# Performance work log

Measured on AMD Instinct MI355X. Metric: run time of the kernel, lower is better.

The kernel has to match this reference:

```python
import jax, jax.numpy as jnp
import numpy as np

EPS = 1e-5


def setup_inputs() -> dict:
    key = jax.random.key(0)
    k1, k2, k3 = jax.random.split(key, 3)
    B, n_per, C_in, C_out = 8, 131072, 32, 64
    N = B * n_per
    coord = jax.random.uniform(k1, (N, 3), dtype=jnp.float32)          # points in unit cube
    feat = jax.random.normal(k2, (N, C_in), dtype=jnp.float32)
    offset = (jnp.arange(1, B + 1, dtype=jnp.int32) * n_per)           # cumulative counts
    W = jax.random.normal(k3, (C_in, C_out), dtype=jnp.float32) * 0.05  # fc weight (no bias)
    gamma = jnp.ones((C_out,), dtype=jnp.float32)
    beta = jnp.zeros((C_out,), dtype=jnp.float32)
    return {"coord": coord, "feat": feat, "offset": offset, "W": W,
            "gamma": gamma, "beta": beta, "grid_size": 0.05}


def reference(coord, feat, offset, W, gamma, beta, grid_size):
    N = coord.shape[0]
    B = offset.shape[0]
    # offset2batch: point i belongs to batch = first b with i < offset[b]
    batch = jnp.searchsorted(offset, jnp.arange(N, dtype=offset.dtype), side="right").astype(jnp.int32)

    # fc -> BatchNorm (training-mode batch stats, biased var) -> ReLU
    h = feat @ W                                                        # [N, C_out]
    mean = h.mean(axis=0)
    var = jnp.mean((h - mean) ** 2, axis=0)
    h = jax.nn.relu((h - mean) * jax.lax.rsqrt(var + EPS) * gamma + beta)

    # start = per-batch min coord (segment_csr 'min' over batch pointer)
    start = jax.ops.segment_min(coord, batch, num_segments=B)           # [B, 3]

    # voxel_grid: integer voxel coords per point, combined with batch into a unique key
    v = jnp.floor((coord - start[batch]) / grid_size).astype(jnp.int32)  # [N, 3] >= 0
    D = v.max(axis=0) + 1                                               # grid extents
    vkey = ((batch * D[0] + v[:, 0]) * D[1] + v[:, 1]) * D[2] + v[:, 2]

    # unique(sorted) + inverse + counts; then segment mean/max by cluster
    uniq, inverse, counts = jnp.unique(vkey, return_inverse=True, return_counts=True)
    inverse = inverse.reshape(-1).astype(jnp.int32)
    M = uniq.shape[0]
    coord_out = jax.ops.segment_sum(coord, inverse, num_segments=M) / counts[:, None].astype(coord.dtype)
    feat_out = jax.ops.segment_max(h, inverse, num_segments=M)

    # batch id of each cluster (constant within cluster) -> new offset
    batch_out = jax.ops.segment_min(batch, inverse, num_segments=M)
    offset_out = jnp.cumsum(jnp.bincount(batch_out, length=B)).astype(offset.dtype)
    return coord_out, feat_out, offset_out, inverse
```

## Files before the change

kernel.cpp:

```cpp
#include <hip/hip_runtime.h>
#include <float.h>

#define EPSV 1e-5f
#define DGRID 21
#define DPROD (21 * 21 * 21)

typedef __attribute__((ext_vector_type(8))) short bf16x8;
typedef __attribute__((ext_vector_type(4))) float f32x4;

__device__ __forceinline__ short f2bf(float x) {
    unsigned u = __float_as_uint(x);
    unsigned r = (u + 0x7FFFu + ((u >> 16) & 1u)) >> 16;
    return (short)r;
}

__device__ __forceinline__ int batch_of(int i, const int* __restrict__ offset, int B) {
    int b = 0;
    while (b < B - 1 && i >= offset[b]) ++b;
    return b;
}

__global__ void k_init(int* startEnc, int B) {
    int tid = threadIdx.x;
    if (tid < B * 3) startEnc[tid] = 0x7FFFFFFF;
}

__global__ void k_start(const float* __restrict__ coord, const int* __restrict__ offset,
                        int* startEnc, int* counts, int KSM, int N, int B) {
    int gtid = blockIdx.x * blockDim.x + threadIdx.x;
    for (int k = gtid; k < KSM; k += gridDim.x * blockDim.x) counts[k] = 0;

    __shared__ int smin[24];
    int t = threadIdx.x;
    if (t < B * 3) smin[t] = 0x7FFFFFFF;
    __syncthreads();
    int base = gtid * 4;
    int curb = -1;
    int m0 = 0x7FFFFFFF, m1 = 0x7FFFFFFF, m2 = 0x7FFFFFFF;
    for (int r = 0; r < 4; ++r) {
        int i = base + r;
        if (i >= N) break;
        int b = batch_of(i, offset, B);
        if (b != curb) {
            if (curb >= 0) {
                atomicMin(&smin[curb * 3 + 0], m0);
                atomicMin(&smin[curb * 3 + 1], m1);
                atomicMin(&smin[curb * 3 + 2], m2);
            }
            curb = b; m0 = m1 = m2 = 0x7FFFFFFF;
        }
        m0 = min(m0, __float_as_int(coord[(size_t)i * 3 + 0]));
        m1 = min(m1, __float_as_int(coord[(size_t)i * 3 + 1]));
        m2 = min(m2, __float_as_int(coord[(size_t)i * 3 + 2]));
    }
    if (curb >= 0) {
        atomicMin(&smin[curb * 3 + 0], m0);
        atomicMin(&smin[curb * 3 + 1], m1);
        atomicMin(&smin[curb * 3 + 2], m2);
    }
    __syncthreads();
    if (t < B * 3 && smin[t] != 0x7FFFFFFF) atomicMin(&startEnc[t], smin[t]);
}

__global__ void k_count(const float* __restrict__ coord, const int* __restrict__ offset,
                        const int* __restrict__ startEnc, const float* __restrict__ gsP,
                        int* counts, int* vkey, int N, int B) {
    int i = blockIdx.x * blockDim.x + threadIdx.x;
    if (i >= N) return;
    float inv_gs = 1.0f / gsP[0];
    int b = batch_of(i, offset, B);
    float s0 = __int_as_float(startEnc[b * 3 + 0]);
    float s1 = __int_as_float(startEnc[b * 3 + 1]);
    float s2 = __int_as_float(startEnc[b * 3 + 2]);
    int vx = min(DGRID - 1, (int)floorf((coord[(size_t)i * 3 + 0] - s0) * inv_gs));
    int vy = min(DGRID - 1, (int)floorf((coord[(size_t)i * 3 + 1] - s1) * inv_gs));
    int vz = min(DGRID - 1, (int)floorf((coord[(size_t)i * 3 + 2] - s2) * inv_gs));
    int k = ((b * DGRID + vx) * DGRID + vy) * DGRID + vz;
    vkey[i] = k;
    atomicAdd(&counts[k], 1);
}

__global__ void k_scan1(const int* __restrict__ counts, int* occPart, int* cntPart, int KSM) {
    __shared__ int so[256], sc[256];
    int t = threadIdx.x;
    int base = blockIdx.x * 1024 + t * 4;
    int o = 0, c = 0;
    for (int r = 0; r < 4; ++r) {
        int k = base + r;
        if (k < KSM) { int cnt = counts[k]; o += (cnt > 0); c += cnt; }
    }
    so[t] = o; sc[t] = c;
    __syncthreads();
    for (int s = 128; s > 0; s >>= 1) {
        if (t < s) { so[t] += so[t + s]; sc[t] += sc[t + s]; }
        __syncthreads();
    }
    if (t == 0) { occPart[blockIdx.x] = so[0]; cntPart[blockIdx.x] = sc[0]; }
}

__global__ void k_scan2(const int* occPart, const int* cntPart,
                        int* occPartEx, int* cntPartEx, int NBLK) {
    __shared__ int so[128], sc[128];
    int t = threadIdx.x;
    int o = (t < NBLK) ? occPart[t] : 0;
    int c = (t < NBLK) ? cntPart[t] : 0;
    so[t] = o; sc[t] = c;
    __syncthreads();
    for (int s = 1; s < 128; s <<= 1) {
        int ao = 0, ac = 0;
        if (t >= s) { ao = so[t - s]; ac = sc[t - s]; }
        __syncthreads();
        so[t] += ao; sc[t] += ac;
        __syncthreads();
    }
    if (t < NBLK) { occPartEx[t] = so[t] - o; cntPartEx[t] = sc[t] - c; }
}

__global__ void k_scan3(const int* __restrict__ counts, const int* occPartEx, const int* cntPartEx,
                        int* occScan, int* cntScan, int* cursor, int* cntC, int* cstartC, int KSM) {
    __shared__ int so[256], sc[256];
    int t = threadIdx.x;
    int base = blockIdx.x * 1024 + t * 4;
    int o[4], c[4];
    int tO = 0, tC = 0;
    for (int r = 0; r < 4; ++r) {
        int k = base + r;
        int cnt = (k < KSM) ? counts[k] : 0;
        o[r] = (cnt > 0); c[r] = cnt;
        tO += o[r]; tC += c[r];
    }
    so[t] = tO; sc[t] = tC;
    __syncthreads();
    for (int s = 1; s < 256; s <<= 1) {
        int ao = 0, ac = 0;
        if (t >= s) { ao = so[t - s]; ac = sc[t - s]; }
        __syncthreads();
        so[t] += ao; sc[t] += ac;
        __syncthreads();
    }
    int exO = so[t] - tO + occPartEx[blockIdx.x];
    int exC = sc[t] - tC + cntPartEx[blockIdx.x];
    for (int r = 0; r < 4; ++r) {
        int k = base + r;
        if (k < KSM) {
            occScan[k] = exO; cntScan[k] = exC; cursor[k] = 0;
            if (c[r] > 0) { cntC[exO] = c[r]; cstartC[exO] = exC; }
            exO += o[r]; exC += c[r];
        }
    }
}

__global__ void k_scatter(const int* __restrict__ vkey,
                          const int* __restrict__ occScan, const int* __restrict__ cntScan,
                          int* cursor, int* plist, float* __restrict__ dout,
                          int N, int B, int M) {
    int i = blockIdx.x * blockDim.x + threadIdx.x;
    if (i >= N) return;
    int k = vkey[i];
    int cidx = occScan[k];
    int pos = cntScan[k] + atomicAdd(&cursor[k], 1);
    plist[pos] = i;
    dout[(size_t)67 * M + B + i] = (float)cidx;
}

__launch_bounds__(64)
__global__ void k_pool(const float* __restrict__ feat, const float* __restrict__ coord,
                       const float* __restrict__ W,
                       const int* __restrict__ cstartC, const int* __restrict__ cntC,
                       const int* __restrict__ plist,
                       float* __restrict__ dout, float* __restrict__ statPart, int M) {
    const int lane = threadIdx.x;
    const int col  = lane & 15;
    const int quad = lane >> 4;
    const int nw = gridDim.x;
    const int gw = blockIdx.x;

    bf16x8 Bf[4];
#pragma unroll
    for (int t = 0; t < 4; ++t) {
#pragma unroll
        for (int j = 0; j < 8; ++j) {
            int k = quad * 8 + j;
            Bf[t][j] = f2bf(W[k * 64 + t * 16 + col]);
        }
    }

    float sumA[4] = {0.f, 0.f, 0.f, 0.f};
    float sqA[4]  = {0.f, 0.f, 0.f, 0.f};

    for (int c0 = gw; c0 < M; c0 += 2 * nw) {
        int c1 = c0 + nw;
        bool has2 = c1 < M;
        if (!has2) c1 = c0;
        int ps0 = cstartC[c0], n0 = cntC[c0];
        int ps1 = cstartC[c1], n1 = cntC[c1];
        int nmax = max(n0, n1);

        float maxA0[4] = {-FLT_MAX, -FLT_MAX, -FLT_MAX, -FLT_MAX};
        float maxA1[4] = {-FLT_MAX, -FLT_MAX, -FLT_MAX, -FLT_MAX};
        float cacc0 = 0.f, cacc1 = 0.f;

        for (int base = 0; base < nmax; base += 16) {
            int m = base + col;
            int idx0 = min(m, n0 - 1);
            int idx1 = min(m, n1 - 1);
            int p0 = plist[ps0 + idx0];
            int p1 = plist[ps1 + idx1];
            const float4* r0p = reinterpret_cast<const float4*>(feat + (size_t)p0 * 32 + quad * 8);
            const float4* r1p = reinterpret_cast<const float4*>(feat + (size_t)p1 * 32 + quad * 8);
            float4 a00 = r0p[0], a01 = r0p[1];
            float4 a10 = r1p[0], a11 = r1p[1];
            if (quad > 0) {
                float v0 = coord[(size_t)p0 * 3 + (quad - 1)];
                float v1 = coord[(size_t)p1 * 3 + (quad - 1)];
                cacc0 += (m < n0) ? v0 : 0.f;
                cacc1 += (m < n1) ? v1 : 0.f;
            }
            bf16x8 Af0, Af1;
            Af0[0] = f2bf(a00.x); Af0[1] = f2bf(a00.y); Af0[2] = f2bf(a00.z); Af0[3] = f2bf(a00.w);
            Af0[4] = f2bf(a01.x); Af0[5] = f2bf(a01.y); Af0[6] = f2bf(a01.z); Af0[7] = f2bf(a01.w);
            Af1[0] = f2bf(a10.x); Af1[1] = f2bf(a10.y); Af1[2] = f2bf(a10.z); Af1[3] = f2bf(a10.w);
            Af1[4] = f2bf(a11.x); Af1[5] = f2bf(a11.y); Af1[6] = f2bf(a11.z); Af1[7] = f2bf(a11.w);
            f32x4 Cz = {0.f, 0.f, 0.f, 0.f};
#pragma unroll
            for (int t = 0; t < 4; ++t) {
                f32x4 v0 = __builtin_amdgcn_mfma_f32_16x16x32_bf16(Af0, Bf[t], Cz, 0, 0, 0);
                f32x4 v1 = __builtin_amdgcn_mfma_f32_16x16x32_bf16(Af1, Bf[t], Cz, 0, 0, 0);
#pragma unroll
                for (int r = 0; r < 4; ++r) {
                    int rowPt = base + quad * 4 + r;
                    maxA0[t] = fmaxf(maxA0[t], v0[r]);
                    maxA1[t] = fmaxf(maxA1[t], v1[r]);
                    float m0 = (rowPt < n0) ? v0[r] : 0.f;
                    sumA[t] += m0; sqA[t] = fmaf(m0, m0, sqA[t]);
                    float m1 = (rowPt < n1 && has2) ? v1[r] : 0.f;
                    sumA[t] += m1; sqA[t] = fmaf(m1, m1, sqA[t]);
                }
            }
        }
        float out0 = 0.f, out1 = 0.f;
#pragma unroll
        for (int t = 0; t < 4; ++t) {
            float v = maxA0[t];
            v = fmaxf(v, __shfl_xor(v, 16, 64));
            v = fmaxf(v, __shfl_xor(v, 32, 64));
            if (quad == t) out0 = v;
            float w = maxA1[t];
            w = fmaxf(w, __shfl_xor(w, 16, 64));
            w = fmaxf(w, __shfl_xor(w, 32, 64));
            if (quad == t) out1 = w;
        }
        dout[(size_t)3 * M + (size_t)c0 * 64 + lane] = out0;
        dout[(size_t)3 * M + (size_t)c1 * 64 + lane] = out1;

        cacc0 += __shfl_xor(cacc0, 1, 64); cacc0 += __shfl_xor(cacc0, 2, 64);
        cacc0 += __shfl_xor(cacc0, 4, 64); cacc0 += __shfl_xor(cacc0, 8, 64);
        cacc1 += __shfl_xor(cacc1, 1, 64); cacc1 += __shfl_xor(cacc1, 2, 64);
        cacc1 += __shfl_xor(cacc1, 4, 64); cacc1 += __shfl_xor(cacc1, 8, 64);
        if (quad > 0 && col == 0) {
            dout[(size_t)c0 * 3 + (quad - 1)] = cacc0 / (float)n0;
            dout[(size_t)c1 * 3 + (quad - 1)] = cacc1 / (float)n1;
        }
    }

    float so = 0.f, qo = 0.f;
#pragma unroll
    for (int t = 0; t < 4; ++t) {
        float s = sumA[t];
        s += __shfl_xor(s, 16, 64);
        s += __shfl_xor(s, 32, 64);
        float q = sqA[t];
        q += __shfl_xor(q, 16, 64);
        q += __shfl_xor(q, 32, 64);
        if (quad == t) { so = s; qo = q; }
    }
    statPart[(size_t)gw * 128 + lane] = so;
    statPart[(size_t)gw * 128 + 64 + lane] = qo;
}

__global__ void k_statred(const float* __restrict__ statPart,
                          const float* __restrict__ gamma, const float* __restrict__ beta,
                          float* bnA, float* bnB, int NB, int N) {
    __shared__ float s1[256], s2[256];
    int c = blockIdx.x;
    int t = threadIdx.x;
    float a = 0.f, b = 0.f;
    for (int bb = t; bb < NB; bb += 256) {
        a += statPart[(size_t)bb * 128 + c];
        b += statPart[(size_t)bb * 128 + 64 + c];
    }
    s1[t] = a; s2[t] = b;
    __syncthreads();
    for (int s = 128; s > 0; s >>= 1) {
        if (t < s) { s1[t] += s1[t + s]; s2[t] += s2[t + s]; }
        __syncthreads();
    }
    if (t == 0) {
        float invN = 1.0f / (float)N;
        float mean = s1[0] * invN;
        float var = s2[0] * invN - mean * mean;
        float aa = gamma[c] / sqrtf(var + EPSV);
        bnA[c] = aa;
        bnB[c] = beta[c] - mean * aa;
    }
}

__global__ void k_final(float* __restrict__ dout, const float* __restrict__ bnA,
                        const float* __restrict__ bnB,
                        const int* __restrict__ occScan, int M, int B) {
    size_t stride = (size_t)gridDim.x * blockDim.x;
    size_t tid0 = (size_t)blockIdx.x * blockDim.x + threadIdx.x;
    size_t totF = (size_t)M * 64;
    for (size_t t = tid0; t < totF; t += stride) {
        int c = (int)(t & 63);
        float v = dout[(size_t)3 * M + t];
        dout[(size_t)3 * M + t] = fmaxf(bnA[c] * v + bnB[c], 0.f);
    }
    if (tid0 < (size_t)B) {
        int val = (tid0 == (size_t)(B - 1)) ? M : occScan[(int)(tid0 + 1) * DPROD];
        dout[(size_t)67 * M + tid0] = (float)val;
    }
}

extern "C" void kernel_launch(void* const* d_in, const int* in_sizes, int n_in,
                              void* d_out, int out_size, void* d_ws, size_t ws_size,
                              hipStream_t stream) {
    const float* coord = (const float*)d_in[0];
    const float* feat  = (const float*)d_in[1];
    const int*   offset = (const int*)d_in[2];
    const float* W     = (const float*)d_in[3];
    const float* gamma = (const float*)d_in[4];
    const float* beta  = (const float*)d_in[5];
    const float* gsP   = (const float*)d_in[6];
    float* dout = (float*)d_out;

    const int N = in_sizes[0] / 3;
    const int B = in_sizes[2];
    const int M = (out_size - B - N) / 67;
    const int KSM = B * DPROD;
    const int NBLK = (KSM + 1023) / 1024;
    const int NBPL = 8192;

    int* wsI = (int*)d_ws;
    int* startEnc  = wsI + 0;
    float* bnA     = (float*)(wsI + 64);
    float* bnB     = (float*)(wsI + 128);
    int* occPart   = wsI + 256;
    int* cntPart   = wsI + 384;
    int* occPartEx = wsI + 512;
    int* cntPartEx = wsI + 640;
    int* counts    = wsI + 1024;
    int* occScan   = counts + KSM;
    int* cntScan   = occScan + KSM;
    int* cursor    = cntScan + KSM;
    int* cntC      = cursor + KSM;
    int* cstartC   = cntC + KSM;
    int* vkey      = cstartC + KSM;
    int* plist     = vkey + N;
    float* statPart = (float*)(plist + N);

    const int TPB = 256;
    int gChunk = (N + 1023) / 1024;
    int gPoint = (N + TPB - 1) / TPB;

    k_init<<<1, 64, 0, stream>>>(startEnc, B);
    k_start<<<gChunk, TPB, 0, stream>>>(coord, offset, startEnc, counts, KSM, N, B);
    k_count<<<gPoint, TPB, 0, stream>>>(coord, offset, startEnc, gsP, counts, vkey, N, B);
    k_scan1<<<NBLK, TPB, 0, stream>>>(counts, occPart, cntPart, KSM);
    k_scan2<<<1, 128, 0, stream>>>(occPart, cntPart, occPartEx, cntPartEx, NBLK);
    k_scan3<<<NBLK, TPB, 0, stream>>>(counts, occPartEx, cntPartEx, occScan, cntScan,
                                      cursor, cntC, cstartC, KSM);
    k_scatter<<<gPoint, TPB, 0, stream>>>(vkey, occScan, cntScan, cursor, plist,
                                          dout, N, B, M);
    k_pool<<<NBPL, 64, 0, stream>>>(feat, coord, W, cstartC, cntC, plist, dout, statPart, M);
    k_statred<<<64, 256, 0, stream>>>(statPart, gamma, beta, bnA, bnB, NBPL, N);
    k_final<<<1024, TPB, 0, stream>>>(dout, bnA, bnB, occScan, M, B);
}
```

Baseline: 390.8 us.

## Pre-permute features to bf16 in scatter order and fold scan2 into scan3

The scatter kernel now converts each point's 32 features to bf16 and writes them contiguously at the point's sorted cluster position. The pool kernel then reads bf16 rows sequentially instead of gathering fp32 rows through plist. This removes the random gather and per-element conversion from the MFMA loop, at the cost of a scattered 64-byte write per point in k_scatter. Separately, the single-block scan2 is merged into scan3: each block rescans the partial sums in shared memory, saving one launch and one round trip through global memory.

```diff
diff --git a/kernel.cpp b/kernel.cpp
--- a/kernel.cpp
+++ b/kernel.cpp
@@ -12,6 +12,9 @@
     unsigned u = __float_as_uint(x);
     unsigned r = (u + 0x7FFFu + ((u >> 16) & 1u)) >> 16;
     return (short)r;
+}
+__device__ __forceinline__ unsigned pk2bf(float a, float b) {
+    return (unsigned)(unsigned short)f2bf(a) | ((unsigned)(unsigned short)f2bf(b) << 16);
 }
 
 __device__ __forceinline__ int batch_of(int i, const int* __restrict__ offset, int B) {
@@ -98,28 +101,31 @@
     if (t == 0) { occPart[blockIdx.x] = so[0]; cntPart[blockIdx.x] = sc[0]; }
 }
 
-__global__ void k_scan2(const int* occPart, const int* cntPart,
-                        int* occPartEx, int* cntPartEx, int NBLK) {
-    __shared__ int so[128], sc[128];
+__global__ void k_scan3(const int* __restrict__ counts,
+                        const int* __restrict__ occPart, const int* __restrict__ cntPart,
+                        int* occScan, int* cntScan, int* cursor, int* cntC, int* cstartC,
+                        int KSM, int NBLK) {
+    __shared__ int so[256], sc[256];
+    __shared__ int po[128], pc[128];
+    __shared__ int exO_s, exC_s;
     int t = threadIdx.x;
-    int o = (t < NBLK) ? occPart[t] : 0;
-    int c = (t < NBLK) ? cntPart[t] : 0;
-    so[t] = o; sc[t] = c;
+
+    int po_v = 0, pc_v = 0;
+    if (t < 128) {
+        po_v = (t < NBLK) ? occPart[t] : 0;
+        pc_v = (t < NBLK) ? cntPart[t] : 0;
+        po[t] = po_v; pc[t] = pc_v;
+    }
     __syncthreads();
     for (int s = 1; s < 128; s <<= 1) {
         int ao = 0, ac = 0;
-        if (t >= s) { ao = so[t - s]; ac = sc[t - s]; }
-        __syncthreads();
-        so[t] += ao; sc[t] += ac;
-        __syncthreads();
-    }
-    if (t < NBLK) { occPartEx[t] = so[t] - o; cntPartEx[t] = sc[t] - c; }
-}
-
-__global__ void k_scan3(const int* __restrict__ counts, const int* occPartEx, const int* cntPartEx,
-                        int* occScan, int* cntScan, int* cursor, int* cntC, int* cstartC, int KSM) {
-    __shared__ int so[256], sc[256];
-    int t = threadIdx.x;
+        if (t < 128 && t >= s) { ao = po[t - s]; ac = pc[t - s]; }
+        __syncthreads();
+        if (t < 128) { po[t] += ao; pc[t] += ac; }
+        __syncthreads();
+    }
+    if (t == (int)blockIdx.x) { exO_s = po[t] - po_v; exC_s = pc[t] - pc_v; }
+
     int base = blockIdx.x * 1024 + t * 4;
     int o[4], c[4];
     int tO = 0, tC = 0;
@@ -138,8 +144,8 @@
         so[t] += ao; sc[t] += ac;
         __syncthreads();
     }
-    int exO = so[t] - tO + occPartEx[blockIdx.x];
-    int exC = sc[t] - tC + cntPartEx[blockIdx.x];
+    int exO = so[t] - tO + exO_s;
+    int exC = sc[t] - tC + exC_s;
     for (int r = 0; r < 4; ++r) {
         int k = base + r;
         if (k < KSM) {
@@ -150,10 +156,10 @@
     }
 }
 
-__global__ void k_scatter(const int* __restrict__ vkey,
+__global__ void k_scatter(const float* __restrict__ feat, const int* __restrict__ vkey,
                           const int* __restrict__ occScan, const int* __restrict__ cntScan,
-                          int* cursor, int* plist, float* __restrict__ dout,
-                          int N, int B, int M) {
+                          int* cursor, int* plist, unsigned short* __restrict__ featP,
+                          float* __restrict__ dout, int N, int B, int M) {
     int i = blockIdx.x * blockDim.x + threadIdx.x;
     if (i >= N) return;
     int k = vkey[i];
@@ -161,10 +167,25 @@
     int pos = cntScan[k] + atomicAdd(&cursor[k], 1);
     plist[pos] = i;
     dout[(size_t)67 * M + B + i] = (float)cidx;
+
+    const float4* src = reinterpret_cast<const float4*>(feat + (size_t)i * 32);
+    uint4 row[4];
+#pragma unroll
+    for (int q = 0; q < 4; ++q) {
+        float4 a = src[q * 2];
+        float4 b = src[q * 2 + 1];
+        row[q].x = pk2bf(a.x, a.y);
+        row[q].y = pk2bf(a.z, a.w);
+        row[q].z = pk2bf(b.x, b.y);
+        row[q].w = pk2bf(b.z, b.w);
+    }
+    uint4* dst = reinterpret_cast<uint4*>(featP + (size_t)pos * 32);
+#pragma unroll
+    for (int q = 0; q < 4; ++q) dst[q] = row[q];
 }
 
 __launch_bounds__(64)
-__global__ void k_pool(const float* __restrict__ feat, const float* __restrict__ coord,
+__global__ void k_pool(const unsigned short* __restrict__ featP, const float* __restrict__ coord,
                        const float* __restrict__ W,
                        const int* __restrict__ cstartC, const int* __restrict__ cntC,
                        const int* __restrict__ plist,
@@ -204,23 +225,16 @@
             int m = base + col;
             int idx0 = min(m, n0 - 1);
             int idx1 = min(m, n1 - 1);
-            int p0 = plist[ps0 + idx0];
-            int p1 = plist[ps1 + idx1];
-            const float4* r0p = reinterpret_cast<const float4*>(feat + (size_t)p0 * 32 + quad * 8);
-            const float4* r1p = reinterpret_cast<const float4*>(feat + (size_t)p1 * 32 + quad * 8);
-            float4 a00 = r0p[0], a01 = r0p[1];
-            float4 a10 = r1p[0], a11 = r1p[1];
+            bf16x8 Af0 = *reinterpret_cast<const bf16x8*>(featP + (size_t)(ps0 + idx0) * 32 + quad * 8);
+            bf16x8 Af1 = *reinterpret_cast<const bf16x8*>(featP + (size_t)(ps1 + idx1) * 32 + quad * 8);
             if (quad > 0) {
+                int p0 = plist[ps0 + idx0];
+                int p1 = plist[ps1 + idx1];
                 float v0 = coord[(size_t)p0 * 3 + (quad - 1)];
                 float v1 = coord[(size_t)p1 * 3 + (quad - 1)];
                 cacc0 += (m < n0) ? v0 : 0.f;
                 cacc1 += (m < n1) ? v1 : 0.f;
             }
-            bf16x8 Af0, Af1;
-            Af0[0] = f2bf(a00.x); Af0[1] = f2bf(a00.y); Af0[2] = f2bf(a00.z); Af0[3] = f2bf(a00.w);
-            Af0[4] = f2bf(a01.x); Af0[5] = f2bf(a01.y); Af0[6] = f2bf(a01.z); Af0[7] = f2bf(a01.w);
-            Af1[0] = f2bf(a10.x); Af1[1] = f2bf(a10.y); Af1[2] = f2bf(a10.z); Af1[3] = f2bf(a10.w);
-            Af1[4] = f2bf(a11.x); Af1[5] = f2bf(a11.y); Af1[6] = f2bf(a11.z); Af1[7] = f2bf(a11.w);
             f32x4 Cz = {0.f, 0.f, 0.f, 0.f};
 #pragma unroll
             for (int t = 0; t < 4; ++t) {
@@ -347,8 +361,6 @@
     float* bnB     = (float*)(wsI + 128);
     int* occPart   = wsI + 256;
     int* cntPart   = wsI + 384;
-    int* occPartEx = wsI + 512;
-    int* cntPartEx = wsI + 640;
     int* counts    = wsI + 1024;
     int* occScan   = counts + KSM;
     int* cntScan   = occScan + KSM;
@@ -358,6 +370,7 @@
     int* vkey      = cstartC + KSM;
     int* plist     = vkey + N;
     float* statPart = (float*)(plist + N);
+    unsigned short* featP = (unsigned short*)(statPart + (size_t)NBPL * 128);
 
     const int TPB = 256;
     int gChunk = (N + 1023) / 1024;
@@ -367,12 +380,11 @@
     k_start<<<gChunk, TPB, 0, stream>>>(coord, offset, startEnc, counts, KSM, N, B);
     k_count<<<gPoint, TPB, 0, stream>>>(coord, offset, startEnc, gsP, counts, vkey, N, B);
     k_scan1<<<NBLK, TPB, 0, stream>>>(counts, occPart, cntPart, KSM);
-    k_scan2<<<1, 128, 0, stream>>>(occPart, cntPart, occPartEx, cntPartEx, NBLK);
-    k_scan3<<<NBLK, TPB, 0, stream>>>(counts, occPartEx, cntPartEx, occScan, cntScan,
-                                      cursor, cntC, cstartC, KSM);
-    k_scatter<<<gPoint, TPB, 0, stream>>>(vkey, occScan, cntScan, cursor, plist,
-                                          dout, N, B, M);
-    k_pool<<<NBPL, 64, 0, stream>>>(feat, coord, W, cstartC, cntC, plist, dout, statPart, M);
+    k_scan3<<<NBLK, TPB, 0, stream>>>(counts, occPart, cntPart, occScan, cntScan,
+                                      cursor, cntC, cstartC, KSM, NBLK);
+    k_scatter<<<gPoint, TPB, 0, stream>>>(feat, vkey, occScan, cntScan, cursor, plist,
+                                          featP, dout, N, B, M);
+    k_pool<<<NBPL, 64, 0, stream>>>(featP, coord, W, cstartC, cntC, plist, dout, statPart, M);
     k_statred<<<64, 256, 0, stream>>>(statPart, gamma, beta, bnA, bnB, NBPL, N);
     k_final<<<1024, TPB, 0, stream>>>(dout, bnA, bnB, occScan, M, B);
 }
```

After: 399.1 us. 2.1% more time.
